# Kernel optimization log

Hardware: AMD Instinct MI355X
Metric: run time of the kernel (lower is better)

The kernel has to match this reference:

```python
import jax, jax.numpy as jnp
import numpy as np

N = 50000      # nodes
E = 1600000    # edges (avg degree 32)
IN, HID, OUT = 32, 32, 10
K = 2          # kernel_size (dim=1, degree=1 open B-spline -> basis (1-u, u))


def setup_inputs() -> dict:
    key = jax.random.key(0)
    ks = jax.random.split(key, 10)
    x = jax.random.normal(ks[0], (N, IN), dtype=jnp.float32)
    edge_index = jax.random.randint(ks[1], (2, E), 0, N, dtype=jnp.int64)
    edge_attr = jax.random.uniform(ks[2], (E, 1), dtype=jnp.float32)  # pseudo-coords in [0,1)
    s1 = 1.0 / np.sqrt(IN * K)
    s2 = 1.0 / np.sqrt(HID * K)
    W1 = jax.random.uniform(ks[3], (K, IN, HID), minval=-s1, maxval=s1, dtype=jnp.float32)
    root1 = jax.random.uniform(ks[4], (IN, HID), minval=-s1, maxval=s1, dtype=jnp.float32)
    b1 = jnp.zeros((HID,), jnp.float32)
    W2 = jax.random.uniform(ks[5], (K, HID, OUT), minval=-s2, maxval=s2, dtype=jnp.float32)
    root2 = jax.random.uniform(ks[6], (HID, OUT), minval=-s2, maxval=s2, dtype=jnp.float32)
    b2 = jnp.zeros((OUT,), jnp.float32)
    return {"x": x, "edge_index": edge_index, "edge_attr": edge_attr,
            "W1": W1, "root1": root1, "b1": b1,
            "W2": W2, "root2": root2, "b2": b2}


def spline_conv(x, edge_index, edge_attr, W, W_root, b):
    # SplineConv, dim=1, kernel_size=2, degree=1, aggr='mean', root_weight, bias.
    # Basis for pseudo u in [0,1): B_0(u) = 1-u, B_1(u) = u.
    src, dst = edge_index[0], edge_index[1]
    u = edge_attr[:, 0]                      # [E]
    h0 = x @ W[0]                            # [N, out] node-level transform, then gather
    h1 = x @ W[1]
    msg = (1.0 - u)[:, None] * h0[src] + u[:, None] * h1[src]   # [E, out]
    n = x.shape[0]
    agg = jax.ops.segment_sum(msg, dst, num_segments=n)
    deg = jax.ops.segment_sum(jnp.ones((src.shape[0],), x.dtype), dst, num_segments=n)
    mean = agg / jnp.maximum(deg, 1.0)[:, None]
    return mean + x @ W_root + b


def reference(x, edge_index, edge_attr, W1, root1, b1, W2, root2, b2):
    # Dropout is identity in eval mode.
    h = jax.nn.relu(spline_conv(x, edge_index, edge_attr, W1, root1, b1))
    h = spline_conv(h, edge_index, edge_attr, W2, root2, b2)
    return jax.nn.log_softmax(h, axis=1)
```

## Files before the change

### kernel.cpp

```cpp
#include <hip/hip_runtime.h>
#include <math.h>

#define GSHIFT 6
#define GSIZE  64
#define NBSZ   1024
#define EPB    4096
#define CAP    3072

#define UDEC1 0.00390625f
#define UDEC2 0.001953125f

__device__ __forceinline__ unsigned bf16rn(float f) {
    unsigned u = __float_as_uint(f);
    return (u + 0x7FFFu + ((u >> 16) & 1u)) >> 16;
}
__device__ __forceinline__ float bfl(unsigned v) { return __uint_as_float(v << 16); }
__device__ __forceinline__ float bfh(unsigned v) { return __uint_as_float(v & 0xFFFF0000u); }

__global__ __launch_bounds__(256) void k_prep(const float* __restrict__ x,
                                              unsigned* __restrict__ x_pk,
                                              int* __restrict__ bcount,
                                              int n, int NB) {
    int t = blockIdx.x * 256 + threadIdx.x;
    if (t < NB) bcount[t] = 0;
    if (t >= n) return;
    const float4* xp = (const float4*)(x + (size_t)t * 32);
    #pragma unroll
    for (int k = 0; k < 4; k++) {
        float4 a = xp[2 * k], c = xp[2 * k + 1];
        uint4 pk;
        pk.x = bf16rn(a.x) | (bf16rn(a.y) << 16);
        pk.y = bf16rn(a.z) | (bf16rn(a.w) << 16);
        pk.z = bf16rn(c.x) | (bf16rn(c.y) << 16);
        pk.w = bf16rn(c.z) | (bf16rn(c.w) << 16);
        *(uint4*)(x_pk + (size_t)t * 16 + k * 4) = pk;
    }
}

__global__ __launch_bounds__(1024) void k_part(const int* __restrict__ src,
                                               const int* __restrict__ dst,
                                               const float* __restrict__ attr,
                                               int* __restrict__ bcount,
                                               unsigned* __restrict__ su,
                                               int E_, int NB) {
    __shared__ int lh[NBSZ];
    __shared__ int lst[NBSZ];
    __shared__ int lcur[NBSZ];
    __shared__ int gbase[NBSZ];
    __shared__ int wsum[16];
    __shared__ __align__(16) unsigned srt[EPB];
    __shared__ unsigned short lbk[EPB];
    int tid = threadIdx.x, lane = tid & 63, w = tid >> 6;
    lh[tid] = 0;
    __syncthreads();
    int base = blockIdx.x * EPB;
    int d[4];
    unsigned rec[4];
    #pragma unroll
    for (int k = 0; k < 4; k++) {
        int e = base + k * 1024 + tid;
        bool val = e < E_;
        int dd = val ? dst[e] : 0;
        int s  = val ? src[e] : 0;
        float a = val ? attr[e] : 0.f;
        d[k] = val ? (dd >> GSHIFT) : -1;
        unsigned uq = (unsigned)(a * 256.0f);
        rec[k] = (unsigned)(s & 0xFFFF) | ((unsigned)(dd & (GSIZE - 1)) << 16) | (uq << 24);
        if (d[k] >= 0) atomicAdd(&lh[d[k]], 1);
    }
    __syncthreads();
    int v = lh[tid];
    int incl = v;
    #pragma unroll
    for (int o = 1; o < 64; o <<= 1) {
        int t2 = __shfl_up(incl, o);
        if (lane >= o) incl += t2;
    }
    if (lane == 63) wsum[w] = incl;
    __syncthreads();
    int woff = 0;
    for (int k = 0; k < w; k++) woff += wsum[k];
    int excl = woff + incl - v;
    lst[tid] = excl;
    lcur[tid] = excl;
    if (tid < NB) gbase[tid] = atomicAdd(&bcount[tid], v);
    __syncthreads();
    #pragma unroll
    for (int k = 0; k < 4; k++) {
        if (d[k] >= 0) {
            int pos = atomicAdd(&lcur[d[k]], 1);
            srt[pos] = rec[k];
            lbk[pos] = (unsigned short)d[k];
        }
    }
    __syncthreads();
    int total = E_ - base; if (total > EPB) total = EPB;
    for (int p = tid; p < total; p += 1024) {
        int b = lbk[p];
        su[(size_t)b * CAP + gbase[b] + (p - lst[b])] = srt[p];
    }
}

__global__ __launch_bounds__(512) void k_fused(const int* __restrict__ bcount,
                                               const unsigned* __restrict__ su,
                                               unsigned* __restrict__ su2,
                                               int* __restrict__ rowptr,
                                               int* __restrict__ deg,
                                               const unsigned* __restrict__ x_pk,
                                               const float* __restrict__ x,
                                               const float* __restrict__ W1,
                                               const float* __restrict__ root1,
                                               const float* __restrict__ b1,
                                               const float* __restrict__ W2,
                                               const float* __restrict__ root2,
                                               unsigned* __restrict__ gg,
                                               float* __restrict__ hr, int n) {
    __shared__ __align__(16) unsigned sorted[CAP];
    __shared__ __align__(16) unsigned accum[GSIZE * 32];
    __shared__ __align__(16) float hl[GSIZE * 32];
    __shared__ int hist[GSIZE], cur[GSIZE], sstart[GSIZE], sdeg[GSIZE];
    __shared__ int stot;

    int b = blockIdx.x, tid = threadIdx.x;
    size_t basee = (size_t)b * CAP;
    int cnt = bcount[b];
    int node0 = b << GSHIFT;

    if (tid < GSIZE) hist[tid] = 0;
    __syncthreads();

    for (int e = tid; e < cnt; e += 512)
        atomicAdd(&hist[(su[basee + e] >> 16) & 63], 1);
    __syncthreads();

    if (tid < 64) {
        int v = hist[tid];
        int pv = (v + 3) & ~3;
        int incl = pv;
        #pragma unroll
        for (int o = 1; o < 64; o <<= 1) {
            int t2 = __shfl_up(incl, o);
            if (tid >= o) incl += t2;
        }
        int excl = incl - pv;
        cur[tid] = excl; sstart[tid] = excl; sdeg[tid] = v;
        int node = node0 + tid;
        if (node < n) { rowptr[node] = (int)basee + excl; deg[node] = v; }
        if (tid == 63) stot = excl + pv;
        for (int p = excl + v; p < excl + pv; p++) sorted[p] = 0;
    }
    __syncthreads();

    for (int e = tid; e < cnt; e += 512) {
        unsigned r = su[basee + e];
        int pos = atomicAdd(&cur[(r >> 16) & 63], 1);
        sorted[pos] = r;
    }
    __syncthreads();

    {
        int tot4 = stot >> 2;
        uint4* dp = (uint4*)(su2 + basee);
        for (int p = tid; p < tot4; p += 512)
            dp[p] = *(const uint4*)(sorted + p * 4);
    }
    {
        int nl = tid >> 3, q = tid & 3, half = (tid >> 2) & 1;
        int st = sstart[nl], dgi = sdeg[nl];
        int endl = st + dgi;
        int q4 = (dgi + 3) >> 2;
        int hq = q4 >> 1, rem = q4 & 1;
        int myq = hq + (half < rem ? 1 : 0);
        int e0 = st + (half * hq + min(half, rem)) * 4;
        float a0[8] = {0,0,0,0,0,0,0,0}, a1[8] = {0,0,0,0,0,0,0,0};
        for (int i = 0; i < myq; i++) {
            int e = e0 + i * 4;
            uint4 rq = *(const uint4*)(sorted + e);
            unsigned rr[4] = {rq.x, rq.y, rq.z, rq.w};
            #pragma unroll
            for (int k = 0; k < 4; k++) {
                bool v = (e + k) < endl;
                unsigned r = rr[k];
                uint4 g = *(const uint4*)(x_pk + (size_t)(r & 0xFFFFu) * 16 + q * 4);
                float wv = v ? 1.f : 0.f;
                float u = v ? fmaf((float)(r >> 24), UDEC1, UDEC2) : 0.f;
                unsigned gw[4] = {g.x, g.y, g.z, g.w};
                #pragma unroll
                for (int m2 = 0; m2 < 4; m2++) {
                    float fl = bfl(gw[m2]), fh = bfh(gw[m2]);
                    a0[2*m2]   = fmaf(wv, fl, a0[2*m2]);
                    a0[2*m2+1] = fmaf(wv, fh, a0[2*m2+1]);
                    a1[2*m2]   = fmaf(u, fl, a1[2*m2]);
                    a1[2*m2+1] = fmaf(u, fh, a1[2*m2+1]);
                }
            }
        }
        #pragma unroll
        for (int k = 0; k < 8; k++) {
            a0[k] += __shfl_xor(a0[k], 4);
            a1[k] += __shfl_xor(a1[k], 4);
        }
        if (half == 0) {
            #pragma unroll
            for (int k = 0; k < 8; k++)
                accum[nl * 32 + q * 8 + k] = bf16rn(a0[k]) | (bf16rn(a1[k]) << 16);
        }
    }
    __syncthreads();

    {
        int nl = tid >> 3, j = tid & 7;
        int node = node0 + nl;
        float invd = 1.0f / fmaxf((float)sdeg[nl], 1.0f);
        float4 hv = *(const float4*)(b1 + 4 * j);
        const float* xrow = x + (size_t)(node < n ? node : 0) * 32;
        for (int i = 0; i < 32; i++) {
            unsigned sp = accum[nl * 32 + i];
            float s0 = bfl(sp) * invd;
            float s1 = bfh(sp) * invd;
            float xi = xrow[i];
            float4 w0 = *(const float4*)(W1 + i * 32 + 4 * j);
            float4 w1 = *(const float4*)(W1 + 1024 + i * 32 + 4 * j);
            float4 rt = *(const float4*)(root1 + i * 32 + 4 * j);
            hv.x = fmaf(s0, w0.x, fmaf(s1, w1.x - w0.x, fmaf(xi, rt.x, hv.x)));
            hv.y = fmaf(s0, w0.y, fmaf(s1, w1.y - w0.y, fmaf(xi, rt.y, hv.y)));
            hv.z = fmaf(s0, w0.z, fmaf(s1, w1.z - w0.z, fmaf(xi, rt.z, hv.z)));
            hv.w = fmaf(s0, w0.w, fmaf(s1, w1.w - w0.w, fmaf(xi, rt.w, hv.w)));
        }
        hv.x = fmaxf(hv.x, 0.f); hv.y = fmaxf(hv.y, 0.f);
        hv.z = fmaxf(hv.z, 0.f); hv.w = fmaxf(hv.w, 0.f);
        *(float4*)(hl + nl * 32 + 4 * j) = hv;
    }
    __syncthreads();

    {
        int nl = tid >> 3, j = tid & 7;
        int node = node0 + nl;
        if (node < n) {
            #pragma unroll
            for (int ci = 0; ci < 2; ci++) {
                int c = j + ci * 8;
                if (c < 10) {
                    float g0 = 0.f, gd = 0.f, gr = 0.f;
                    for (int i = 0; i < 32; i++) {
                        float hi = hl[nl * 32 + i];
                        float wa = W2[i * 10 + c];
                        g0 = fmaf(hi, wa, g0);
                        gd = fmaf(hi, W2[320 + i * 10 + c] - wa, gd);
                        gr = fmaf(hi, root2[i * 10 + c], gr);
                    }
                    gg[(size_t)node * 16 + c] = bf16rn(g0) | (bf16rn(gd) << 16);
                    hr[(size_t)node * 10 + c] = gr;
                } else {
                    gg[(size_t)node * 16 + c] = 0;
                }
            }
        }
    }
}

__global__ __launch_bounds__(256) void k_agg2(const int* __restrict__ rowptr,
                                              const int* __restrict__ deg,
                                              const unsigned* __restrict__ su2,
                                              const unsigned* __restrict__ gg,
                                              const float* __restrict__ hr,
                                              const float* __restrict__ b2,
                                              float* __restrict__ out, int n) {
    int lane = threadIdx.x & 63;
    int node = (blockIdx.x * 4 + (threadIdx.x >> 6)) * 4 + (lane >> 4);
    int qt = (lane >> 2) & 3;
    int q  = lane & 3;
    if (node >= n) return;
    int start = rowptr[node], dgi = deg[node], end = start + dgi;
    int q4 = (dgi + 3) >> 2;
    int qb = q4 >> 2, rem = q4 & 3;
    int myq = qb + (qt < rem ? 1 : 0);
    int e0 = start + (qt * qb + min(qt, rem)) * 4;
    float acc[4] = {0, 0, 0, 0};
    for (int i = 0; i < myq; i++) {
        int e = e0 + i * 4;
        uint4 rq = *(const uint4*)(su2 + e);
        unsigned rr[4] = {rq.x, rq.y, rq.z, rq.w};
        #pragma unroll
        for (int k = 0; k < 4; k++) {
            bool v = (e + k) < end;
            unsigned r = rr[k];
            uint4 g = *(const uint4*)(gg + (size_t)(r & 0xFFFFu) * 16 + q * 4);
            float wv = v ? 1.f : 0.f;
            float u = v ? fmaf((float)(r >> 24), UDEC1, UDEC2) : 0.f;
            acc[0] = fmaf(wv, bfl(g.x), fmaf(u, bfh(g.x), acc[0]));
            acc[1] = fmaf(wv, bfl(g.y), fmaf(u, bfh(g.y), acc[1]));
            acc[2] = fmaf(wv, bfl(g.z), fmaf(u, bfh(g.z), acc[2]));
            acc[3] = fmaf(wv, bfl(g.w), fmaf(u, bfh(g.w), acc[3]));
        }
    }
    #pragma unroll
    for (int k = 0; k < 4; k++) {
        acc[k] += __shfl_xor(acc[k], 4);
        acc[k] += __shfl_xor(acc[k], 8);
    }
    float invd = 1.0f / fmaxf((float)dgi, 1.0f);
    int c0 = q * 4;
    float lg[4];
    float m = -INFINITY;
    #pragma unroll
    for (int k = 0; k < 4; k++) {
        int c = c0 + k;
        if (c < 10) {
            lg[k] = fmaf(acc[k], invd, hr[(size_t)node * 10 + c] + b2[c]);
            m = fmaxf(m, lg[k]);
        } else lg[k] = -INFINITY;
    }
    m = fmaxf(m, __shfl_xor(m, 1));
    m = fmaxf(m, __shfl_xor(m, 2));
    float ex = 0.f;
    #pragma unroll
    for (int k = 0; k < 4; k++)
        if (c0 + k < 10) ex += __expf(lg[k] - m);
    ex += __shfl_xor(ex, 1);
    ex += __shfl_xor(ex, 2);
    float lse = m + __logf(ex);
    if (qt == 0 && c0 < 10) {
        *(float2*)(out + (size_t)node * 10 + c0) =
            make_float2(lg[0] - lse, lg[1] - lse);
        if (c0 + 2 < 10)
            *(float2*)(out + (size_t)node * 10 + c0 + 2) =
                make_float2(lg[2] - lse, lg[3] - lse);
    }
}

extern "C" void kernel_launch(void* const* d_in, const int* in_sizes, int n_in,
                              void* d_out, int out_size, void* d_ws, size_t ws_size,
                              hipStream_t stream) {
    const float* x     = (const float*)d_in[0];
    const int*   ei    = (const int*)d_in[1];
    const float* attr  = (const float*)d_in[2];
    const float* W1    = (const float*)d_in[3];
    const float* root1 = (const float*)d_in[4];
    const float* b1    = (const float*)d_in[5];
    const float* W2    = (const float*)d_in[6];
    const float* root2 = (const float*)d_in[7];
    const float* b2    = (const float*)d_in[8];
    float* out = (float*)d_out;

    int N_ = in_sizes[0] / 32;
    int E_ = in_sizes[1] / 2;
    const int* src = ei;
    const int* dst = ei + E_;
    int NB = (N_ + GSIZE - 1) >> GSHIFT;
    int NP = (E_ + EPB - 1) / EPB;

    char* ws = (char*)d_ws;
    size_t off = 0;
    auto alloc = [&](size_t bytes) -> void* {
        void* p = ws + off;
        off += (bytes + 255) & ~(size_t)255;
        return p;
    };
    int*      bcount = (int*)     alloc((size_t)NB * 4);
    unsigned* su     = (unsigned*)alloc(((size_t)NB * CAP + 64) * 4);
    unsigned* su2    = (unsigned*)alloc(((size_t)NB * CAP + 64) * 4);
    int*      rowptr = (int*)     alloc((size_t)N_ * 4);
    int*      deg    = (int*)     alloc((size_t)N_ * 4);
    unsigned* x_pk   = (unsigned*)alloc((size_t)N_ * 16 * 4);
    unsigned* gg     = (unsigned*)alloc((size_t)N_ * 16 * 4);
    float*    hr     = (float*)   alloc((size_t)N_ * 10 * 4);

    int prep_blocks = (N_ > NB ? N_ : NB);
    k_prep <<<(prep_blocks + 255) / 256, 256, 0, stream>>>(x, x_pk, bcount, N_, NB);
    k_part <<<NP, 1024, 0, stream>>>(src, dst, attr, bcount, su, E_, NB);
    k_fused<<<NB, 512, 0, stream>>>(bcount, su, su2, rowptr, deg, x_pk, x,
                                    W1, root1, b1, W2, root2, gg, hr, N_);
    k_agg2 <<<(N_ + 15) / 16, 256, 0, stream>>>(rowptr, deg, su2, gg, hr, b2, out, N_);
}
```

Baseline: 93.28 us.

## Stage layer weights in LDS as packed bf16 and vectorize edge loads

Each block now stages W1 (as packed bf16 w0/w1-w0 pairs), root1, W2 (packed), root2 and b1 in shared memory at kernel start instead of reading them from global memory inside the per-node dense loops. The hidden activations are stored as packed bf16 pairs, and the histogram and scatter passes read the edge records as uint4. This cuts global/L1 traffic in the dense transforms and the number of load instructions in the sorting passes. In exchange it adds more LDS use per block, which may lower occupancy, and extra bf16 rounding of the weights and hidden activations, which reduces accuracy.

```diff
diff --git a/kernel.cpp b/kernel.cpp
--- a/kernel.cpp
+++ b/kernel.cpp
@@ -117,7 +117,12 @@
                                                float* __restrict__ hr, int n) {
     __shared__ __align__(16) unsigned sorted[CAP];
     __shared__ __align__(16) unsigned accum[GSIZE * 32];
-    __shared__ __align__(16) float hl[GSIZE * 32];
+    __shared__ __align__(16) unsigned hlp[GSIZE * 16];
+    __shared__ __align__(16) unsigned sw01[1024];
+    __shared__ __align__(16) float sRt[1024];
+    __shared__ unsigned sAD[320];
+    __shared__ float sR2[320];
+    __shared__ float sB1[32];
     __shared__ int hist[GSIZE], cur[GSIZE], sstart[GSIZE], sdeg[GSIZE];
     __shared__ int stot;
 
@@ -127,10 +132,26 @@
     int node0 = b << GSHIFT;
 
     if (tid < GSIZE) hist[tid] = 0;
-    __syncthreads();
-
-    for (int e = tid; e < cnt; e += 512)
-        atomicAdd(&hist[(su[basee + e] >> 16) & 63], 1);
+    for (int i = tid; i < 1024; i += 512) {
+        float w0 = W1[i];
+        sw01[i] = bf16rn(w0) | (bf16rn(W1[1024 + i] - w0) << 16);
+        sRt[i] = root1[i];
+    }
+    if (tid < 320) {
+        float a0 = W2[tid];
+        sAD[tid] = bf16rn(a0) | (bf16rn(W2[320 + tid] - a0) << 16);
+        sR2[tid] = root2[tid];
+    }
+    if (tid < 32) sB1[tid] = b1[tid];
+    __syncthreads();
+
+    for (int e = tid * 4; e < cnt; e += 2048) {
+        uint4 r4 = *(const uint4*)(su + basee + e);
+        unsigned rr[4] = {r4.x, r4.y, r4.z, r4.w};
+        #pragma unroll
+        for (int k = 0; k < 4; k++)
+            if (e + k < cnt) atomicAdd(&hist[(rr[k] >> 16) & 63], 1);
+    }
     __syncthreads();
 
     if (tid < 64) {
@@ -151,10 +172,17 @@
     }
     __syncthreads();
 
-    for (int e = tid; e < cnt; e += 512) {
-        unsigned r = su[basee + e];
-        int pos = atomicAdd(&cur[(r >> 16) & 63], 1);
-        sorted[pos] = r;
+    for (int e = tid * 4; e < cnt; e += 2048) {
+        uint4 r4 = *(const uint4*)(su + basee + e);
+        unsigned rr[4] = {r4.x, r4.y, r4.z, r4.w};
+        #pragma unroll
+        for (int k = 0; k < 4; k++) {
+            if (e + k < cnt) {
+                unsigned r = rr[k];
+                int pos = atomicAdd(&cur[(r >> 16) & 63], 1);
+                sorted[pos] = r;
+            }
+        }
     }
     __syncthreads();
 
@@ -212,24 +240,24 @@
         int nl = tid >> 3, j = tid & 7;
         int node = node0 + nl;
         float invd = 1.0f / fmaxf((float)sdeg[nl], 1.0f);
-        float4 hv = *(const float4*)(b1 + 4 * j);
+        float4 hv = make_float4(sB1[4*j], sB1[4*j+1], sB1[4*j+2], sB1[4*j+3]);
         const float* xrow = x + (size_t)(node < n ? node : 0) * 32;
         for (int i = 0; i < 32; i++) {
             unsigned sp = accum[nl * 32 + i];
             float s0 = bfl(sp) * invd;
             float s1 = bfh(sp) * invd;
             float xi = xrow[i];
-            float4 w0 = *(const float4*)(W1 + i * 32 + 4 * j);
-            float4 w1 = *(const float4*)(W1 + 1024 + i * 32 + 4 * j);
-            float4 rt = *(const float4*)(root1 + i * 32 + 4 * j);
-            hv.x = fmaf(s0, w0.x, fmaf(s1, w1.x - w0.x, fmaf(xi, rt.x, hv.x)));
-            hv.y = fmaf(s0, w0.y, fmaf(s1, w1.y - w0.y, fmaf(xi, rt.y, hv.y)));
-            hv.z = fmaf(s0, w0.z, fmaf(s1, w1.z - w0.z, fmaf(xi, rt.z, hv.z)));
-            hv.w = fmaf(s0, w0.w, fmaf(s1, w1.w - w0.w, fmaf(xi, rt.w, hv.w)));
+            uint4 wp = *(const uint4*)(sw01 + i * 32 + 4 * j);
+            float4 rt = *(const float4*)(sRt + i * 32 + 4 * j);
+            hv.x = fmaf(s0, bfl(wp.x), fmaf(s1, bfh(wp.x), fmaf(xi, rt.x, hv.x)));
+            hv.y = fmaf(s0, bfl(wp.y), fmaf(s1, bfh(wp.y), fmaf(xi, rt.y, hv.y)));
+            hv.z = fmaf(s0, bfl(wp.z), fmaf(s1, bfh(wp.z), fmaf(xi, rt.z, hv.z)));
+            hv.w = fmaf(s0, bfl(wp.w), fmaf(s1, bfh(wp.w), fmaf(xi, rt.w, hv.w)));
         }
         hv.x = fmaxf(hv.x, 0.f); hv.y = fmaxf(hv.y, 0.f);
         hv.z = fmaxf(hv.z, 0.f); hv.w = fmaxf(hv.w, 0.f);
-        *(float4*)(hl + nl * 32 + 4 * j) = hv;
+        hlp[nl * 16 + 2 * j]     = bf16rn(hv.x) | (bf16rn(hv.y) << 16);
+        hlp[nl * 16 + 2 * j + 1] = bf16rn(hv.z) | (bf16rn(hv.w) << 16);
     }
     __syncthreads();
 
@@ -242,12 +270,15 @@
                 int c = j + ci * 8;
                 if (c < 10) {
                     float g0 = 0.f, gd = 0.f, gr = 0.f;
-                    for (int i = 0; i < 32; i++) {
-                        float hi = hl[nl * 32 + i];
-                        float wa = W2[i * 10 + c];
-                        g0 = fmaf(hi, wa, g0);
-                        gd = fmaf(hi, W2[320 + i * 10 + c] - wa, gd);
-                        gr = fmaf(hi, root2[i * 10 + c], gr);
+                    for (int i2 = 0; i2 < 16; i2++) {
+                        unsigned hp = hlp[nl * 16 + i2];
+                        float h0 = bfl(hp), h1 = bfh(hp);
+                        int i = 2 * i2;
+                        unsigned wa = sAD[i * 10 + c];
+                        unsigned wb = sAD[(i + 1) * 10 + c];
+                        g0 = fmaf(h0, bfl(wa), fmaf(h1, bfl(wb), g0));
+                        gd = fmaf(h0, bfh(wa), fmaf(h1, bfh(wb), gd));
+                        gr = fmaf(h0, sR2[i * 10 + c], fmaf(h1, sR2[(i + 1) * 10 + c], gr));
                     }
                     gg[(size_t)node * 16 + c] = bf16rn(g0) | (bf16rn(gd) << 16);
                     hr[(size_t)node * 10 + c] = gr;
```

Result: faster. 75.64 us (-18.9%).
